# Kernel optimization log

Hardware: AMD Instinct MI355X
Metric: run time of the kernel (lower is better)

## Reference

```python
import jax, jax.numpy as jnp
import numpy as np

NEG = -9e15
ALPHA = 0.2  # LeakyReLU slope


def xavier(key, shape, gain=1.414):
    fan_in, fan_out = shape[-2], shape[-1]
    bound = gain * np.sqrt(6.0 / (fan_in + fan_out))
    return jax.random.uniform(key, shape, jnp.float32, -bound, bound)


def setup_inputs() -> dict:
    key = jax.random.key(0)
    ks = jax.random.split(key, 8)
    N, D_IN, HID, OUT, H = 4096, 128, 64, 64, 4
    x = jax.random.normal(ks[0], (N, D_IN), jnp.float32)
    adj = jax.random.randint(ks[1], (N, N), 0, 2, jnp.int32)
    # layer 0: in=D_IN, out=HID, heads=H
    W0 = xavier(ks[2], (H, D_IN, HID))
    a0 = xavier(ks[3], (H, 2 * HID, 1))
    # layer 1: in=HID*H, out=HID, heads=H
    W1 = xavier(ks[4], (H, HID * H, HID))
    a1 = xavier(ks[5], (H, 2 * HID, 1))
    # layer 2: in=HID*H, out=OUT, heads=1
    W2 = xavier(ks[6], (1, HID * H, OUT))
    a2 = xavier(ks[7], (1, 2 * OUT, 1))
    return {"x": x, "adj": adj, "W0": W0, "a0": a0, "W1": W1, "a1": a1, "W2": W2, "a2": a2}


def gat_layer(x, adj_mask, W, a):
    # x: [N, D], W: [H, D, O], a: [H, 2O, 1]
    O = W.shape[-1]
    h = jnp.einsum('nd,hdo->hno', x, W)                      # [H, N, O]
    a_l, a_r = a[:, :O, 0], a[:, O:, 0]                      # [H, O] each
    e_l = jnp.einsum('hno,ho->hn', h, a_l)                   # a^T[Wh_i||Wh_j] split
    e_r = jnp.einsum('hno,ho->hn', h, a_r)
    e = e_l[:, :, None] + e_r[:, None, :]                    # [H, N, N]
    e = jnp.where(e > 0, e, ALPHA * e)                       # LeakyReLU
    att = jnp.where(adj_mask[None], e, NEG)
    att = jax.nn.softmax(att, axis=-1)                       # dropout skipped (eval)
    out = jnp.einsum('hnm,hmo->hno', att, h)                 # [H, N, O]
    N = x.shape[0]
    return out.transpose(1, 0, 2).reshape(N, -1)             # [N, H*O]


def reference(x, adj, W0, a0, W1, a1, W2, a2):
    adj_mask = adj > 0
    h = gat_layer(x, adj_mask, W0, a0)
    h = jax.nn.elu(h)
    h = gat_layer(h, adj_mask, W1, a1)
    h = jax.nn.elu(h)
    h = gat_layer(h, adj_mask, W2, a2)
    return h
```

## Files before the change

### kernel.cpp

```cpp
#include <hip/hip_runtime.h>

#define LOG2E 1.4426950408889634f

typedef float  f32x4 __attribute__((ext_vector_type(4)));
typedef int    i32x4 __attribute__((ext_vector_type(4)));
typedef short  s16x8 __attribute__((ext_vector_type(8)));
typedef unsigned long long u64x2 __attribute__((ext_vector_type(2)));

static __device__ __forceinline__ float exp2_fast(float x) {
#if __has_builtin(__builtin_amdgcn_exp2f)
    return __builtin_amdgcn_exp2f(x);
#else
    return exp2f(x);
#endif
}
static __device__ __forceinline__ unsigned short bf16_rne(float f) {
    unsigned u = __float_as_uint(f);
    u += 0x7FFFu + ((u >> 16) & 1u);
    return (unsigned short)(u >> 16);
}
static __device__ __forceinline__ int sbfe1(unsigned w, int pos) {
#if __has_builtin(__builtin_amdgcn_sbfe)
    return __builtin_amdgcn_sbfe((int)w, pos, 1);
#else
    return (int)(w << (31 - pos)) >> 31;
#endif
}
static __device__ __forceinline__ unsigned pack_hi16(unsigned u1, unsigned u0) {
#if __has_builtin(__builtin_amdgcn_perm)
    return __builtin_amdgcn_perm(u1, u0, 0x07060302u);
#else
    return (u0 >> 16) | (u1 & 0xFFFF0000u);
#endif
}

__global__ __launch_bounds__(256) void prep_all(
    const float* __restrict__ xf, const int* __restrict__ adj,
    const float* __restrict__ W0, const float* __restrict__ W1,
    const float* __restrict__ W2,
    unsigned short* __restrict__ xc, unsigned long long* __restrict__ bits,
    unsigned short* __restrict__ W0t, unsigned short* __restrict__ W1t,
    unsigned short* __restrict__ W2t, unsigned* __restrict__ MxU)
{
    const int b = blockIdx.x, tid = threadIdx.x;
    if (b < 16384) {
        const int w = tid >> 6, lane = tid & 63;
        const int base = b * 1024 + w * 256;
        unsigned long long m[4];
#pragma unroll
        for (int r = 0; r < 4; ++r)
            m[r] = __ballot(adj[base + r * 64 + lane] != 0);
        if (lane == 0) {
            u64x2 lo = {m[0], m[1]}, hi = {m[2], m[3]};
            *(u64x2*)(bits + (base >> 6))     = lo;
            *(u64x2*)(bits + (base >> 6) + 2) = hi;
        }
    } else if (b < 18432) {
        int i = (b - 16384) * 256 + tid;
        xc[i] = bf16_rne(xf[i]);
    } else {
        int gid = (b - 18432) * 256 + tid;
        if (gid < 32768) {
            int h = gid >> 13, d = (gid >> 6) & 127, o = gid & 63;
            W0t[(h * 64 + o) * 128 + d] = bf16_rne(W0[gid]);
        } else if (gid < 98304) {
            int g = gid - 32768;
            int h = g >> 14, d = (g >> 6) & 255, o = g & 63;
            W1t[(h * 64 + o) * 256 + d] = bf16_rne(W1[g]);
        } else if (gid < 114688) {
            int g = gid - 98304;
            int d = g >> 6, o = g & 63;
            W2t[o * 256 + d] = bf16_rne(W2[g]);
        } else if (gid < 114700) {
            MxU[gid - 114688] = 0x007FFFFFu;
        }
    }
}

__global__ __launch_bounds__(128) void gemm_elr(
    const unsigned short* __restrict__ X, int K,
    const unsigned short* __restrict__ Wt,
    const float* __restrict__ a,
    unsigned short* __restrict__ hT,
    float* __restrict__ el2, float* __restrict__ er2,
    unsigned* __restrict__ MxU)
{
    const int lane = threadIdx.x & 63, w = threadIdx.x >> 6;
    const int c = lane & 15, q = lane >> 4;
    const int h = blockIdx.y;
    const int nb = blockIdx.x * 32 + w * 16;
    const unsigned short* xrow = X + (size_t)(nb + c) * K + q * 8;
    const unsigned short* wb   = Wt + ((size_t)h * 64 + c) * K + q * 8;

    f32x4 acc[4] = {{0,0,0,0},{0,0,0,0},{0,0,0,0},{0,0,0,0}};
    for (int kk = 0; kk < K; kk += 32) {
        s16x8 af = *(const s16x8*)(xrow + kk);
#pragma unroll
        for (int j = 0; j < 4; ++j) {
            s16x8 bf = *(const s16x8*)(wb + (size_t)(j * 16) * K + kk);
            acc[j] = __builtin_amdgcn_mfma_f32_16x16x32_bf16(af, bf, acc[j], 0, 0, 0);
        }
    }
#pragma unroll
    for (int j = 0; j < 4; ++j) {
        unsigned d0 = (unsigned)bf16_rne(acc[j][0]) | ((unsigned)bf16_rne(acc[j][1]) << 16);
        unsigned d1 = (unsigned)bf16_rne(acc[j][2]) | ((unsigned)bf16_rne(acc[j][3]) << 16);
        unsigned short* dst = hT + ((size_t)h * 64 + j * 16 + c) * 4096 + nb + q * 4;
        ((unsigned*)dst)[0] = d0;
        ((unsigned*)dst)[1] = d1;
    }
    const float* ab = a + h * 128;
    float elr[4] = {0,0,0,0}, err[4] = {0,0,0,0};
#pragma unroll
    for (int j = 0; j < 4; ++j) {
        float al = ab[j * 16 + c];
        float ar = ab[64 + j * 16 + c];
#pragma unroll
        for (int r = 0; r < 4; ++r) {
            elr[r] = fmaf(al, acc[j][r], elr[r]);
            err[r] = fmaf(ar, acc[j][r], err[r]);
        }
    }
#pragma unroll
    for (int m = 1; m <= 8; m <<= 1) {
#pragma unroll
        for (int r = 0; r < 4; ++r) {
            elr[r] += __shfl_xor(elr[r], m, 64);
            err[r] += __shfl_xor(err[r], m, 64);
        }
    }
    if (c == 0) {
#pragma unroll
        for (int r = 0; r < 4; ++r) {
            int n = nb + q * 4 + r;
            el2[h * 4096 + n] = elr[r] * LOG2E;
            er2[h * 4096 + n] = err[r] * LOG2E;
        }
    }
    float mm = fmaxf(fmaxf(err[0], err[1]), fmaxf(err[2], err[3]));
    mm = fmaxf(mm, __shfl_xor(mm, 16, 64));
    mm = fmaxf(mm, __shfl_xor(mm, 32, 64));
    if (lane == 0) {
        unsigned u = __float_as_uint(mm * LOG2E);
        unsigned key = (u & 0x80000000u) ? ~u : (u | 0x80000000u);
        atomicMax(MxU + h, key);
    }
}

__global__ __launch_bounds__(256) void att_kernel(
    const unsigned short* __restrict__ hT,
    const float* __restrict__ el2g, const float* __restrict__ er2g,
    const unsigned* __restrict__ MxU,
    const unsigned long long* __restrict__ bits,
    float* __restrict__ accP, float* __restrict__ lP,
    int H, int KPS, int HO)
{
    __shared__ unsigned short ldsH[2][64 * 128];
    __shared__ float ldsE[2][256];
    const int tid = threadIdx.x;
    const int lane = tid & 63, w = tid >> 6;
    const int c = lane & 15, q = lane >> 4, q8 = q * 8;
    const int h = blockIdx.y, ks = blockIdx.z;
    const int nb = blockIdx.x * 64 + w * 16;
    const int rowA = nb + c;

    unsigned kM = MxU[h];
    float M2 = __uint_as_float((kM & 0x80000000u) ? (kM & 0x7FFFFFFFu) : ~kM);
    float e2 = el2g[h * 4096 + rowA];
    float xx = e2 + M2;
    float C2 = fmaxf(xx, 0.2f * xx);
    const float Al = exp2_fast(xx - C2);
    const float Bl = exp2_fast(fmaf(0.2f, xx, -C2));

    const char* bitrow = (const char*)bits + (size_t)rowA * 512 + (size_t)(KPS >> 3) * ks;
    const unsigned short* hTh = hT + (size_t)h * 64 * 4096;
    const float* erh = er2g + h * 4096;
    const int tiles = KPS >> 7;
    const int kbase = ks * KPS;
    const int col = tid & 127, hi = tid >> 7;

    auto STAGE = [&](int buf, int mabs_) {
#pragma unroll
        for (int i = 0; i < 4; ++i) {
            int cidx = i * 256 + tid;
            int o = cidx >> 4, g = cidx & 15;
            const unsigned short* sp =
                hTh + (size_t)o * 4096 + mabs_ + ((g ^ (o & 7)) << 3);
            unsigned short* dp = &ldsH[buf][(i * 256 + (tid & ~63)) << 3];
            __builtin_amdgcn_global_load_lds(
                (const __attribute__((address_space(1))) void*)sp,
                (__attribute__((address_space(3))) void*)dp, 16, 0, 0);
        }
    };

    s16x8 ones = {0,0,0,0,0,0,0,0};
    if (c == 0) {
#pragma unroll
        for (int i = 0; i < 8; ++i) ones[i] = (short)0x3F80;
    }
    f32x4 acc[4] = {{0,0,0,0},{0,0,0,0},{0,0,0,0},{0,0,0,0}};
    f32x4 accl = {0,0,0,0};

    STAGE(0, kbase);
    {
        float ee = erh[kbase + col] - M2;
        float xin = hi ? 0.2f * ee : ee;
        ldsE[0][2 * col + hi] = exp2_fast(xin);
    }
    i32x4 bA = *(const i32x4*)(bitrow);
    __syncthreads();

    for (int t = 0; t < tiles; ++t) {
        const int cur = t & 1, nxt = cur ^ 1;
        const bool more = (t + 1 < tiles);
        const unsigned short* Hc = ldsH[cur];
        const float* Ec = ldsE[cur];

        const f32x4* ep0 = (const f32x4*)(Ec + 2 * q8);
        f32x4 nv0 = ep0[0], nv1 = ep0[1], nv2 = ep0[2], nv3 = ep0[3];

        float ern = 0.f;
        if (more) {
            const int mn = kbase + (t + 1) * 128;
            STAGE(nxt, mn);
            ern = erh[mn + col];
        }
        int bw[4] = {bA[0], bA[1], bA[2], bA[3]};
        if (more) bA = *(const i32x4*)(bitrow + (t + 1) * 16);

#pragma unroll
        for (int cc = 0; cc < 4; ++cc) {
            f32x4 ev0 = nv0, ev1 = nv1, ev2 = nv2, ev3 = nv3;
            if (cc < 3) {
                const f32x4* epn = (const f32x4*)(Ec + 2 * ((cc + 1) * 32 + q8));
                nv0 = epn[0]; nv1 = epn[1]; nv2 = epn[2]; nv3 = epn[3];
            }
            const int kl = cc * 32 + q8;
            const unsigned word = (unsigned)bw[cc];
            unsigned pd[4];
#pragma unroll
            for (int jj = 0; jj < 4; ++jj) {
                f32x4 ev = (jj == 0) ? ev0 : (jj == 1) ? ev1 : (jj == 2) ? ev2 : ev3;
                float p0 = fmaxf(Al * ev[0], Bl * ev[1]);
                float p1 = fmaxf(Al * ev[2], Bl * ev[3]);
                unsigned u0 = __float_as_uint(p0) & (unsigned)sbfe1(word, q8 + 2 * jj);
                unsigned u1 = __float_as_uint(p1) & (unsigned)sbfe1(word, q8 + 2 * jj + 1);
                pd[jj] = pack_hi16(u1, u0);
            }
            union { unsigned u[4]; s16x8 s; } afu;
            afu.u[0] = pd[0]; afu.u[1] = pd[1]; afu.u[2] = pd[2]; afu.u[3] = pd[3];
            s16x8 af = afu.s;
            const int klx = kl ^ ((c & 7) << 3);
            const unsigned short* lb = Hc + c * 128 + klx;
            __builtin_amdgcn_s_setprio(1);
#pragma unroll
            for (int j = 0; j < 4; ++j) {
                s16x8 bf = *(const s16x8*)(lb + (size_t)(j * 16) * 128);
                acc[j] = __builtin_amdgcn_mfma_f32_16x16x32_bf16(af, bf, acc[j], 0, 0, 0);
            }
            accl = __builtin_amdgcn_mfma_f32_16x16x32_bf16(af, ones, accl, 0, 0, 0);
            __builtin_amdgcn_s_setprio(0);
        }

        if (more) {
            float ee = ern - M2;
            float xin = hi ? 0.2f * ee : ee;
            ldsE[nxt][2 * col + hi] = exp2_fast(xin);
        }
        __syncthreads();
    }

    float ls[4];
#pragma unroll
    for (int r = 0; r < 4; ++r) ls[r] = __shfl(accl[r], lane & 48, 64);

    float* ap = accP + ((size_t)ks * 4096 + nb + q * 4) * HO + h * 64 + c;
#pragma unroll
    for (int r = 0; r < 4; ++r)
#pragma unroll
        for (int j = 0; j < 4; ++j)
            ap[(size_t)r * HO + j * 16] = acc[j][r];
    if (c == 0) {
#pragma unroll
        for (int r = 0; r < 4; ++r)
            lP[((size_t)ks * H + h) * 4096 + nb + q * 4 + r] = ls[r];
    }
}

__global__ __launch_bounds__(256) void comb_kernel(
    const float* __restrict__ accP, const float* __restrict__ lP,
    unsigned short* __restrict__ outb, float* __restrict__ outf,
    int KS, int H, int lgHO, int do_elu)
{
    const int idx = blockIdx.x * 256 + threadIdx.x;
    const int HO = 1 << lgHO;
    const int n = idx >> lgHO, col = idx & (HO - 1), h = col >> 6;
    float s = 0.f, l = 0.f;
    for (int ks = 0; ks < KS; ++ks) {
        s += accP[((size_t)ks * 4096 + n) * HO + col];
        l += lP[((size_t)ks * H + h) * 4096 + n];
    }
    float v = s / l;
    if (do_elu && v < 0.f) v = exp2_fast(v * LOG2E) - 1.f;
    if (outf) outf[idx] = v;
    else      outb[idx] = bf16_rne(v);
}

extern "C" void kernel_launch(void* const* d_in, const int* in_sizes, int n_in,
                              void* d_out, int out_size, void* d_ws, size_t ws_size,
                              hipStream_t stream)
{
    (void)in_sizes; (void)n_in; (void)out_size; (void)ws_size;
    const float* x   = (const float*)d_in[0];
    const int*   adj = (const int*)d_in[1];
    const float* W0  = (const float*)d_in[2];
    const float* a0  = (const float*)d_in[3];
    const float* W1  = (const float*)d_in[4];
    const float* a1  = (const float*)d_in[5];
    const float* W2  = (const float*)d_in[6];
    const float* a2  = (const float*)d_in[7];

    char* p = (char*)d_ws;
    unsigned long long* bits = (unsigned long long*)(p + 0x000000);
    unsigned short* hT  = (unsigned short*)(p + 0x200000);
    unsigned short* X12 = (unsigned short*)(p + 0x400000);
    unsigned short* Xc  = (unsigned short*)(p + 0x600000);
    unsigned short* W0t = (unsigned short*)(p + 0x700000);
    unsigned short* W1t = (unsigned short*)(p + 0x710000);
    unsigned short* W2t = (unsigned short*)(p + 0x730000);
    float*    el2  = (float*)(p + 0x738000);
    float*    er2  = (float*)(p + 0x748000);
    unsigned* MxU  = (unsigned*)(p + 0x758000);
    float*    accP = (float*)(p + 0x760000);
    float*    lP   = (float*)(p + 0x1760000);

    prep_all<<<18881, 256, 0, stream>>>(x, adj, W0, W1, W2, Xc, bits,
                                        W0t, W1t, W2t, MxU);

    gemm_elr<<<dim3(128, 4), 128, 0, stream>>>(Xc, 128, W0t, a0, hT, el2, er2, MxU + 0);
    att_kernel<<<dim3(64, 4, 4), 256, 0, stream>>>(hT, el2, er2, MxU + 0, bits, accP, lP, 4, 1024, 256);
    comb_kernel<<<4096, 256, 0, stream>>>(accP, lP, X12, nullptr, 4, 4, 8, 1);

    gemm_elr<<<dim3(128, 4), 128, 0, stream>>>(X12, 256, W1t, a1, hT, el2, er2, MxU + 4);
    att_kernel<<<dim3(64, 4, 4), 256, 0, stream>>>(hT, el2, er2, MxU + 4, bits, accP, lP, 4, 1024, 256);
    comb_kernel<<<4096, 256, 0, stream>>>(accP, lP, X12, nullptr, 4, 4, 8, 1);

    gemm_elr<<<dim3(128, 1), 128, 0, stream>>>(X12, 256, W2t, a2, hT, el2, er2, MxU + 8);
    att_kernel<<<dim3(64, 1, 16), 256, 0, stream>>>(hT, el2, er2, MxU + 8, bits, accP, lP, 1, 256, 64);
    comb_kernel<<<1024, 256, 0, stream>>>(accP, lP, nullptr, (float*)d_out, 16, 1, 6, 0);
}
```

Measured before the change: 229.2 us.

## Process two row sets per attention block to reuse staged H tiles

```diff
diff --git a/kernel.cpp b/kernel.cpp
--- a/kernel.cpp
+++ b/kernel.cpp
@@ -3,6 +3,7 @@
 #define LOG2E 1.4426950408889634f
 
 typedef float  f32x4 __attribute__((ext_vector_type(4)));
+typedef float  f32x2 __attribute__((ext_vector_type(2)));
 typedef int    i32x4 __attribute__((ext_vector_type(4)));
 typedef short  s16x8 __attribute__((ext_vector_type(8)));
 typedef unsigned long long u64x2 __attribute__((ext_vector_type(2)));
@@ -147,6 +148,7 @@
     }
 }
 
+template <int SETS>
 __global__ __launch_bounds__(256) void att_kernel(
     const unsigned short* __restrict__ hT,
     const float* __restrict__ el2g, const float* __restrict__ er2g,
@@ -156,28 +158,36 @@
     int H, int KPS, int HO)
 {
     __shared__ unsigned short ldsH[2][64 * 128];
-    __shared__ float ldsE[2][256];
+    __shared__ float ldsE[2][2][128];
     const int tid = threadIdx.x;
     const int lane = tid & 63, w = tid >> 6;
     const int c = lane & 15, q = lane >> 4, q8 = q * 8;
     const int h = blockIdx.y, ks = blockIdx.z;
-    const int nb = blockIdx.x * 64 + w * 16;
-    const int rowA = nb + c;
+    const int nb = blockIdx.x * (64 * SETS) + w * 16;
 
     unsigned kM = MxU[h];
     float M2 = __uint_as_float((kM & 0x80000000u) ? (kM & 0x7FFFFFFFu) : ~kM);
-    float e2 = el2g[h * 4096 + rowA];
-    float xx = e2 + M2;
-    float C2 = fmaxf(xx, 0.2f * xx);
-    const float Al = exp2_fast(xx - C2);
-    const float Bl = exp2_fast(fmaf(0.2f, xx, -C2));
-
-    const char* bitrow = (const char*)bits + (size_t)rowA * 512 + (size_t)(KPS >> 3) * ks;
+
+    f32x2 Av[SETS], Bv[SETS];
+    const char* bitrow[SETS];
+#pragma unroll
+    for (int s = 0; s < SETS; ++s) {
+        int rowA = nb + s * 64 + c;
+        float e2 = el2g[h * 4096 + rowA];
+        float xx = e2 + M2;
+        float C2 = fmaxf(xx, 0.2f * xx);
+        float Al = exp2_fast(xx - C2);
+        float Bl = exp2_fast(fmaf(0.2f, xx, -C2));
+        Av[s] = (f32x2){Al, Al};
+        Bv[s] = (f32x2){Bl, Bl};
+        bitrow[s] = (const char*)bits + (size_t)rowA * 512 + (size_t)(KPS >> 3) * ks;
+    }
+
     const unsigned short* hTh = hT + (size_t)h * 64 * 4096;
     const float* erh = er2g + h * 4096;
     const int tiles = KPS >> 7;
     const int kbase = ks * KPS;
-    const int col = tid & 127, hi = tid >> 7;
+    const int colE = tid & 127, hiE = tid >> 7;
 
     auto STAGE = [&](int buf, int mabs_) {
 #pragma unroll
@@ -198,92 +208,127 @@
 #pragma unroll
         for (int i = 0; i < 8; ++i) ones[i] = (short)0x3F80;
     }
-    f32x4 acc[4] = {{0,0,0,0},{0,0,0,0},{0,0,0,0},{0,0,0,0}};
-    f32x4 accl = {0,0,0,0};
+    f32x4 acc[SETS][4];
+    f32x4 accl[SETS];
+#pragma unroll
+    for (int s = 0; s < SETS; ++s) {
+        accl[s] = (f32x4){0,0,0,0};
+#pragma unroll
+        for (int j = 0; j < 4; ++j) acc[s][j] = (f32x4){0,0,0,0};
+    }
 
     STAGE(0, kbase);
     {
-        float ee = erh[kbase + col] - M2;
-        float xin = hi ? 0.2f * ee : ee;
-        ldsE[0][2 * col + hi] = exp2_fast(xin);
-    }
-    i32x4 bA = *(const i32x4*)(bitrow);
+        float ee = erh[kbase + colE] - M2;
+        float xin = hiE ? 0.2f * ee : ee;
+        ldsE[0][hiE][colE] = exp2_fast(xin);
+    }
+    i32x4 bA[SETS];
+#pragma unroll
+    for (int s = 0; s < SETS; ++s) bA[s] = *(const i32x4*)(bitrow[s]);
     __syncthreads();
 
     for (int t = 0; t < tiles; ++t) {
         const int cur = t & 1, nxt = cur ^ 1;
         const bool more = (t + 1 < tiles);
         const unsigned short* Hc = ldsH[cur];
-        const float* Ec = ldsE[cur];
-
-        const f32x4* ep0 = (const f32x4*)(Ec + 2 * q8);
-        f32x4 nv0 = ep0[0], nv1 = ep0[1], nv2 = ep0[2], nv3 = ep0[3];
+        const float* EcA = ldsE[cur][0];
+        const float* EcB = ldsE[cur][1];
 
         float ern = 0.f;
         if (more) {
             const int mn = kbase + (t + 1) * 128;
             STAGE(nxt, mn);
-            ern = erh[mn + col];
-        }
-        int bw[4] = {bA[0], bA[1], bA[2], bA[3]};
-        if (more) bA = *(const i32x4*)(bitrow + (t + 1) * 16);
+            ern = erh[mn + colE];
+        }
+        int bw[SETS][4];
+#pragma unroll
+        for (int s = 0; s < SETS; ++s) {
+            bw[s][0] = bA[s][0]; bw[s][1] = bA[s][1];
+            bw[s][2] = bA[s][2]; bw[s][3] = bA[s][3];
+        }
+        if (more) {
+#pragma unroll
+            for (int s = 0; s < SETS; ++s)
+                bA[s] = *(const i32x4*)(bitrow[s] + (t + 1) * 16);
+        }
 
 #pragma unroll
         for (int cc = 0; cc < 4; ++cc) {
-            f32x4 ev0 = nv0, ev1 = nv1, ev2 = nv2, ev3 = nv3;
-            if (cc < 3) {
-                const f32x4* epn = (const f32x4*)(Ec + 2 * ((cc + 1) * 32 + q8));
-                nv0 = epn[0]; nv1 = epn[1]; nv2 = epn[2]; nv3 = epn[3];
-            }
             const int kl = cc * 32 + q8;
-            const unsigned word = (unsigned)bw[cc];
-            unsigned pd[4];
-#pragma unroll
-            for (int jj = 0; jj < 4; ++jj) {
-                f32x4 ev = (jj == 0) ? ev0 : (jj == 1) ? ev1 : (jj == 2) ? ev2 : ev3;
-                float p0 = fmaxf(Al * ev[0], Bl * ev[1]);
-                float p1 = fmaxf(Al * ev[2], Bl * ev[3]);
-                unsigned u0 = __float_as_uint(p0) & (unsigned)sbfe1(word, q8 + 2 * jj);
-                unsigned u1 = __float_as_uint(p1) & (unsigned)sbfe1(word, q8 + 2 * jj + 1);
-                pd[jj] = pack_hi16(u1, u0);
-            }
-            union { unsigned u[4]; s16x8 s; } afu;
-            afu.u[0] = pd[0]; afu.u[1] = pd[1]; afu.u[2] = pd[2]; afu.u[3] = pd[3];
-            s16x8 af = afu.s;
+            const f32x4* eap = (const f32x4*)(EcA + kl);
+            const f32x4* ebp = (const f32x4*)(EcB + kl);
+            f32x4 eA0 = eap[0], eA1 = eap[1];
+            f32x4 eB0 = ebp[0], eB1 = ebp[1];
             const int klx = kl ^ ((c & 7) << 3);
             const unsigned short* lb = Hc + c * 128 + klx;
+            s16x8 bf[4];
+#pragma unroll
+            for (int j = 0; j < 4; ++j)
+                bf[j] = *(const s16x8*)(lb + (size_t)(j * 16) * 128);
+
+            s16x8 af[SETS];
+#pragma unroll
+            for (int s = 0; s < SETS; ++s) {
+                const unsigned word = (unsigned)bw[s][cc];
+                unsigned pd[4];
+#pragma unroll
+                for (int jj = 0; jj < 4; ++jj) {
+                    f32x2 ea = (jj == 0) ? eA0.xy : (jj == 1) ? eA0.zw
+                             : (jj == 2) ? eA1.xy : eA1.zw;
+                    f32x2 eb = (jj == 0) ? eB0.xy : (jj == 1) ? eB0.zw
+                             : (jj == 2) ? eB1.xy : eB1.zw;
+                    f32x2 pa = Av[s] * ea;
+                    f32x2 pb = Bv[s] * eb;
+                    float p0 = fmaxf(pa.x, pb.x);
+                    float p1 = fmaxf(pa.y, pb.y);
+                    unsigned u0 = __float_as_uint(p0) & (unsigned)sbfe1(word, q8 + 2 * jj);
+                    unsigned u1 = __float_as_uint(p1) & (unsigned)sbfe1(word, q8 + 2 * jj + 1);
+                    pd[jj] = pack_hi16(u1, u0);
+                }
+                union { unsigned u[4]; s16x8 s8; } afu;
+                afu.u[0] = pd[0]; afu.u[1] = pd[1];
+                afu.u[2] = pd[2]; afu.u[3] = pd[3];
+                af[s] = afu.s8;
+            }
             __builtin_amdgcn_s_setprio(1);
 #pragma unroll
-            for (int j = 0; j < 4; ++j) {
-                s16x8 bf = *(const s16x8*)(lb + (size_t)(j * 16) * 128);
-                acc[j] = __builtin_amdgcn_mfma_f32_16x16x32_bf16(af, bf, acc[j], 0, 0, 0);
+            for (int s = 0; s < SETS; ++s) {
+#pragma unroll
+                for (int j = 0; j < 4; ++j)
+                    acc[s][j] = __builtin_amdgcn_mfma_f32_16x16x32_bf16(
+                        af[s], bf[j], acc[s][j], 0, 0, 0);
+                accl[s] = __builtin_amdgcn_mfma_f32_16x16x32_bf16(
+                    af[s], ones, accl[s], 0, 0, 0);
             }
-            accl = __builtin_amdgcn_mfma_f32_16x16x32_bf16(af, ones, accl, 0, 0, 0);
             __builtin_amdgcn_s_setprio(0);
         }
 
         if (more) {
             float ee = ern - M2;
-            float xin = hi ? 0.2f * ee : ee;
-            ldsE[nxt][2 * col + hi] = exp2_fast(xin);
+            float xin = hiE ? 0.2f * ee : ee;
+            ldsE[nxt][hiE][colE] = exp2_fast(xin);
         }
         __syncthreads();
     }
 
-    float ls[4];
-#pragma unroll
-    for (int r = 0; r < 4; ++r) ls[r] = __shfl(accl[r], lane & 48, 64);
-
-    float* ap = accP + ((size_t)ks * 4096 + nb + q * 4) * HO + h * 64 + c;
-#pragma unroll
-    for (int r = 0; r < 4; ++r)
-#pragma unroll
-        for (int j = 0; j < 4; ++j)
-            ap[(size_t)r * HO + j * 16] = acc[j][r];
-    if (c == 0) {
+#pragma unroll
+    for (int s = 0; s < SETS; ++s) {
+        float ls[4];
+#pragma unroll
+        for (int r = 0; r < 4; ++r) ls[r] = __shfl(accl[s][r], lane & 48, 64);
+
+        float* ap = accP + ((size_t)ks * 4096 + nb + s * 64 + q * 4) * HO + h * 64 + c;
 #pragma unroll
         for (int r = 0; r < 4; ++r)
-            lP[((size_t)ks * H + h) * 4096 + nb + q * 4 + r] = ls[r];
+#pragma unroll
+            for (int j = 0; j < 4; ++j)
+                ap[(size_t)r * HO + j * 16] = acc[s][j][r];
+        if (c == 0) {
+#pragma unroll
+            for (int r = 0; r < 4; ++r)
+                lP[((size_t)ks * H + h) * 4096 + nb + s * 64 + q * 4 + r] = ls[r];
+        }
     }
 }
 
@@ -338,14 +383,14 @@
                                         W0t, W1t, W2t, MxU);
 
     gemm_elr<<<dim3(128, 4), 128, 0, stream>>>(Xc, 128, W0t, a0, hT, el2, er2, MxU + 0);
-    att_kernel<<<dim3(64, 4, 4), 256, 0, stream>>>(hT, el2, er2, MxU + 0, bits, accP, lP, 4, 1024, 256);
+    att_kernel<2><<<dim3(32, 4, 4), 256, 0, stream>>>(hT, el2, er2, MxU + 0, bits, accP, lP, 4, 1024, 256);
     comb_kernel<<<4096, 256, 0, stream>>>(accP, lP, X12, nullptr, 4, 4, 8, 1);
 
     gemm_elr<<<dim3(128, 4), 128, 0, stream>>>(X12, 256, W1t, a1, hT, el2, er2, MxU + 4);
-    att_kernel<<<dim3(64, 4, 4), 256, 0, stream>>>(hT, el2, er2, MxU + 4, bits, accP, lP, 4, 1024, 256);
+    att_kernel<2><<<dim3(32, 4, 4), 256, 0, stream>>>(hT, el2, er2, MxU + 4, bits, accP, lP, 4, 1024, 256);
     comb_kernel<<<4096, 256, 0, stream>>>(accP, lP, X12, nullptr, 4, 4, 8, 1);
 
     gemm_elr<<<dim3(128, 1), 128, 0, stream>>>(X12, 256, W2t, a2, hT, el2, er2, MxU + 8);
-    att_kernel<<<dim3(64, 1, 16), 256, 0, stream>>>(hT, el2, er2, MxU + 8, bits, accP, lP, 1, 256, 64);
+    att_kernel<1><<<dim3(64, 1, 16), 256, 0, stream>>>(hT, el2, er2, MxU + 8, bits, accP, lP, 1, 256, 64);
     comb_kernel<<<1024, 256, 0, stream>>>(accP, lP, nullptr, (float*)d_out, 16, 1, 6, 0);
 }
```

After: 232.5 us. About the same (+1.5%).
